# Optimization experiments

Measured on AMD Instinct MI355X. Metric: run time of the kernel, lower is better.

Reference implementation:

```python
import jax, jax.numpy as jnp
import numpy as np


def setup_inputs() -> dict:
    key = jax.random.key(0)
    k1, k2, k3 = jax.random.split(key, 3)
    B, N, C, H, W = 4, 6, 80, 16, 44
    image_features = jax.random.normal(k1, (B * N, C, H, W), dtype=jnp.float32)
    # eye + small perturbation keeps the 3x3 intrinsics block invertible
    intrinsics = jnp.eye(4, dtype=jnp.float32) + 0.1 * jax.random.normal(k2, (B, N, 4, 4), dtype=jnp.float32)
    extrinsics = jnp.eye(4, dtype=jnp.float32) + 0.1 * jax.random.normal(k3, (B, N, 4, 4), dtype=jnp.float32)
    return {"image_features": image_features, "intrinsics": intrinsics,
            "extrinsics": extrinsics, "depth_bins": 59}


def reference(image_features, intrinsics, extrinsics, depth_bins):
    BN, C, H, W = image_features.shape
    N = intrinsics.shape[1]
    B = BN // N
    dt = image_features.dtype
    depths = jnp.linspace(0.1, 1.0, depth_bins).astype(dt)  # (D,)
    feats = image_features.reshape(B, N, C, H, W)

    # pixel homogeneous coords, matching torch meshgrid(indexing='ij') + flatten
    yy, xx = jnp.meshgrid(jnp.arange(H), jnp.arange(W), indexing='ij')
    xy1 = jnp.stack([xx.ravel(), yy.ravel(), jnp.ones(H * W)], axis=0).astype(dt)  # (3, HW)

    K_inv = jnp.linalg.inv(intrinsics[:, :, :3, :3])            # (B,N,3,3)
    rays = jnp.einsum('bnij,jp->bnip', K_inv, xy1)              # (B,N,3,HW)

    # softmax over spatial dim (dim=3 of (B,N,C,HW) in the torch code)
    depth_probs = jax.nn.softmax(feats.reshape(B, N, C, H * W), axis=3)

    # In the original, only the LAST 4 channels of the (4C+1)-channel homogeneous
    # volume enter the extrinsic matmul: the [x,y,z] coords of channel C-1 plus 1.
    d_last = depth_probs[:, :, -1]                              # (B,N,HW)
    # (B,N,3,HW,D) = rays * (prob * depth)
    pts = rays[..., None] * (d_last[:, :, None, :, None] * depths)

    R = extrinsics[:, :, :3, :3]                                # (B,N,3,3)
    t = extrinsics[:, :, :3, 3]                                 # (B,N,3)
    world = jnp.einsum('bnij,bnjpd->bnipd', R, pts) + t[:, :, :, None, None]
    world = world.reshape(B, N, 3, H, W, depth_bins)

    feats_rep = jnp.broadcast_to(feats[..., None], (B, N, C, H, W, depth_bins))
    return jnp.concatenate([world, feats_rep], axis=2)         # (B,N,3+C,H,W,D)
```

## Files before the change

### kernel.cpp

```cpp
#include <hip/hip_runtime.h>


#define BB 4
#define NN 6
#define CC 80
#define HH 16
#define WW 44
#define DD 59
#define BN (BB*NN)
#define PP (HH*WW)
#define CHO (CC+3)
#define WD (WW*DD)

#define WS_DLAST (BN*12)

__device__ inline float waveMax(float v) {
#pragma unroll
    for (int o = 32; o; o >>= 1) v = fmaxf(v, __shfl_xor(v, o));
    return v;
}
__device__ inline float waveSum(float v) {
#pragma unroll
    for (int o = 32; o; o >>= 1) v += __shfl_xor(v, o);
    return v;
}

__global__ __launch_bounds__(256) void lss_prep(const float* __restrict__ feats,
                                                const float* __restrict__ intr,
                                                const float* __restrict__ extr,
                                                float* __restrict__ ws) {
    const int bn = blockIdx.x;
    const int tid = threadIdx.x;
    float* Mt = ws + bn * 12;
    float* dlast = ws + WS_DLAST + (size_t)bn * PP;
    const float* f = feats + ((size_t)bn * CC + (CC - 1)) * PP;

    __shared__ float sred[4];
    __shared__ float s_max, s_sum;

    float m = -1e30f;
    for (int p = tid; p < PP; p += 256) m = fmaxf(m, f[p]);
    m = waveMax(m);
    if ((tid & 63) == 0) sred[tid >> 6] = m;
    __syncthreads();
    if (tid == 0) s_max = fmaxf(fmaxf(sred[0], sred[1]), fmaxf(sred[2], sred[3]));
    __syncthreads();
    const float mm = s_max;

    float s = 0.f;
    for (int p = tid; p < PP; p += 256) s += expf(f[p] - mm);
    s = waveSum(s);
    if ((tid & 63) == 0) sred[tid >> 6] = s;
    __syncthreads();
    if (tid == 0) s_sum = sred[0] + sred[1] + sred[2] + sred[3];
    __syncthreads();
    const float inv = 1.0f / s_sum;

    for (int p = tid; p < PP; p += 256) dlast[p] = expf(f[p] - mm) * inv;

    if (tid == 0) {
        const float* K = intr + bn * 16;
        float a = K[0], b = K[1], c = K[2];
        float d = K[4], e = K[5], ff = K[6];
        float g = K[8], h = K[9], i = K[10];
        float det = a * (e * i - ff * h) - b * (d * i - ff * g) + c * (d * h - e * g);
        float id = 1.0f / det;
        float kinv[9] = {
            (e * i - ff * h) * id, (c * h - b * i) * id, (b * ff - c * e) * id,
            (ff * g - d * i) * id, (a * i - c * g) * id, (c * d - a * ff) * id,
            (d * h - e * g) * id,  (b * g - a * h) * id, (a * e - b * d) * id
        };
        const float* E = extr + bn * 16;
#pragma unroll
        for (int r = 0; r < 3; ++r) {
#pragma unroll
            for (int cc2 = 0; cc2 < 3; ++cc2) {
                float acc = 0.f;
#pragma unroll
                for (int k = 0; k < 3; ++k) acc += E[r * 4 + k] * kinv[k * 3 + cc2];
                Mt[r * 3 + cc2] = acc;
            }
            Mt[9 + r] = E[r * 4 + 3];
        }
    }
}

__global__ __launch_bounds__(256) void lss_write(const float* __restrict__ feats,
                                                 const float* __restrict__ ws,
                                                 float* __restrict__ out) {
    const int blk = blockIdx.x;
    const int h = blk & (HH - 1);
    const int chbn = blk >> 4;
    const int ch = chbn % CHO;
    const int bn = chbn / CHO;
    const int tid = threadIdx.x;

    __shared__ float valw[WW];
    __shared__ float s_t;

    const float* Mt = ws + bn * 12;
    const bool isWorld = (ch < 3);

    if (isWorld) {
        if (tid < WW) {
            const float* dlast = ws + WS_DLAST + (size_t)bn * PP + h * WW;
            float x = (float)tid, y = (float)h;
            float ray = Mt[ch * 3 + 0] * x + Mt[ch * 3 + 1] * y + Mt[ch * 3 + 2];
            valw[tid] = ray * dlast[tid];
        }
        if (tid == 0) s_t = Mt[9 + ch];
    } else {
        if (tid < WW) {
            const float* frow = feats + (((size_t)bn * CC + (ch - 3)) * HH + h) * WW;
            valw[tid] = frow[tid];
        }
        if (tid == 0) s_t = 0.f;
    }
    __syncthreads();

    const float tval = s_t;
    float4* orow = (float4*)(out + (size_t)blk * WD);

    for (int q = tid; q < WD / 4; q += 256) {
        int base = q * 4;
        int w = base / DD;
        int d = base - w * DD;
        float4 v;
        float* pv = &v.x;
#pragma unroll
        for (int k = 0; k < 4; ++k) {
            float val = valw[w];
            if (isWorld) val = val * (0.1f + d * (0.9f / 58.f)) + tval;
            pv[k] = val;
            if (++d == DD) { d = 0; ++w; }
        }
        orow[q] = v;
    }
}

extern "C" void kernel_launch(void* const* d_in, const int* in_sizes, int n_in,
                              void* d_out, int out_size, void* d_ws, size_t ws_size,
                              hipStream_t stream) {
    const float* feats = (const float*)d_in[0];
    const float* intr  = (const float*)d_in[1];
    const float* extr  = (const float*)d_in[2];
    float* ws  = (float*)d_ws;
    float* out = (float*)d_out;

    lss_prep<<<BN, 256, 0, stream>>>(feats, intr, extr, ws);
    lss_write<<<BN * CHO * HH, 256, 0, stream>>>(feats, ws, out);
}
```

Before: 78.67 us.

## Fuse prep and write kernels, recompute softmax per world block, use nontemporal stores

Merges the softmax/matrix prep kernel into the output-writing kernel. Each world-channel block recomputes the softmax of the last feature channel and its camera matrix row locally. Blocks now cover half the image rows instead of one row, and per-thread index/scale tables are precomputed once and reused across rows. Output goes out with nontemporal vector stores. The launch and the workspace round trip go away, at the cost of redundant softmax work in world blocks and fewer, larger blocks.

```diff
diff --git a/kernel.cpp b/kernel.cpp
--- a/kernel.cpp
+++ b/kernel.cpp
@@ -11,8 +11,12 @@
 #define PP (HH*WW)
 #define CHO (CC+3)
 #define WD (WW*DD)
+#define NQ4 (WD/4)
+#define HSPLIT 2
+#define HLOC (HH/HSPLIT)
+#define DSTEP (0.9f/58.f)
 
-#define WS_DLAST (BN*12)
+typedef float fx4 __attribute__((ext_vector_type(4)));
 
 __device__ inline float waveMax(float v) {
 #pragma unroll
@@ -25,116 +29,141 @@
     return v;
 }
 
-__global__ __launch_bounds__(256) void lss_prep(const float* __restrict__ feats,
-                                                const float* __restrict__ intr,
-                                                const float* __restrict__ extr,
-                                                float* __restrict__ ws) {
-    const int bn = blockIdx.x;
-    const int tid = threadIdx.x;
-    float* Mt = ws + bn * 12;
-    float* dlast = ws + WS_DLAST + (size_t)bn * PP;
-    const float* f = feats + ((size_t)bn * CC + (CC - 1)) * PP;
+__global__ __launch_bounds__(256) void lss_all(const float* __restrict__ feats,
+                                               const float* __restrict__ intr,
+                                               const float* __restrict__ extr,
+                                               float* __restrict__ out) {
+    const int blk  = blockIdx.x;
+    const int hs   = blk & (HSPLIT - 1);
+    const int chbn = blk >> 1;
+    const int ch   = chbn % CHO;
+    const int bn   = chbn / CHO;
+    const int tid  = threadIdx.x;
+    const bool world = (ch < 3);
 
+    __shared__ float sf[PP];
+    __shared__ float valw[HLOC][WW + 1];
     __shared__ float sred[4];
-    __shared__ float s_max, s_sum;
+    __shared__ float sbc[2];
 
-    float m = -1e30f;
-    for (int p = tid; p < PP; p += 256) m = fmaxf(m, f[p]);
-    m = waveMax(m);
-    if ((tid & 63) == 0) sred[tid >> 6] = m;
-    __syncthreads();
-    if (tid == 0) s_max = fmaxf(fmaxf(sred[0], sred[1]), fmaxf(sred[2], sred[3]));
-    __syncthreads();
-    const float mm = s_max;
+    float tval = 0.f;
 
-    float s = 0.f;
-    for (int p = tid; p < PP; p += 256) s += expf(f[p] - mm);
-    s = waveSum(s);
-    if ((tid & 63) == 0) sred[tid >> 6] = s;
-    __syncthreads();
-    if (tid == 0) s_sum = sred[0] + sred[1] + sred[2] + sred[3];
-    __syncthreads();
-    const float inv = 1.0f / s_sum;
+    if (world) {
+        const float* f = feats + ((size_t)bn * CC + (CC - 1)) * PP;
+        float m = -1e30f;
+        for (int p = tid; p < PP; p += 256) { float v = f[p]; sf[p] = v; m = fmaxf(m, v); }
+        m = waveMax(m);
+        if ((tid & 63) == 0) sred[tid >> 6] = m;
+        __syncthreads();
+        if (tid == 0) sbc[0] = fmaxf(fmaxf(sred[0], sred[1]), fmaxf(sred[2], sred[3]));
+        __syncthreads();
+        const float mm = sbc[0];
+        float s = 0.f;
+        for (int p = tid; p < PP; p += 256) { float e = expf(sf[p] - mm); sf[p] = e; s += e; }
+        s = waveSum(s);
+        if ((tid & 63) == 0) sred[tid >> 6] = s;
+        __syncthreads();
+        if (tid == 0) sbc[1] = sred[0] + sred[1] + sred[2] + sred[3];
+        __syncthreads();
+        const float inv = 1.0f / sbc[1];
 
-    for (int p = tid; p < PP; p += 256) dlast[p] = expf(f[p] - mm) * inv;
-
-    if (tid == 0) {
         const float* K = intr + bn * 16;
         float a = K[0], b = K[1], c = K[2];
         float d = K[4], e = K[5], ff = K[6];
-        float g = K[8], h = K[9], i = K[10];
-        float det = a * (e * i - ff * h) - b * (d * i - ff * g) + c * (d * h - e * g);
+        float g = K[8], h9 = K[9], i9 = K[10];
+        float det = a * (e * i9 - ff * h9) - b * (d * i9 - ff * g) + c * (d * h9 - e * g);
         float id = 1.0f / det;
         float kinv[9] = {
-            (e * i - ff * h) * id, (c * h - b * i) * id, (b * ff - c * e) * id,
-            (ff * g - d * i) * id, (a * i - c * g) * id, (c * d - a * ff) * id,
-            (d * h - e * g) * id,  (b * g - a * h) * id, (a * e - b * d) * id
+            (e * i9 - ff * h9) * id, (c * h9 - b * i9) * id, (b * ff - c * e) * id,
+            (ff * g - d * i9) * id,  (a * i9 - c * g) * id,  (c * d - a * ff) * id,
+            (d * h9 - e * g) * id,   (b * g - a * h9) * id,  (a * e - b * d) * id
         };
         const float* E = extr + bn * 16;
-#pragma unroll
-        for (int r = 0; r < 3; ++r) {
-#pragma unroll
-            for (int cc2 = 0; cc2 < 3; ++cc2) {
-                float acc = 0.f;
-#pragma unroll
-                for (int k = 0; k < 3; ++k) acc += E[r * 4 + k] * kinv[k * 3 + cc2];
-                Mt[r * 3 + cc2] = acc;
-            }
-            Mt[9 + r] = E[r * 4 + 3];
+        float M0 = E[ch * 4 + 0] * kinv[0] + E[ch * 4 + 1] * kinv[3] + E[ch * 4 + 2] * kinv[6];
+        float M1 = E[ch * 4 + 0] * kinv[1] + E[ch * 4 + 1] * kinv[4] + E[ch * 4 + 2] * kinv[7];
+        float M2 = E[ch * 4 + 0] * kinv[2] + E[ch * 4 + 1] * kinv[5] + E[ch * 4 + 2] * kinv[8];
+        tval = E[ch * 4 + 3];
+
+        for (int t2 = tid; t2 < HLOC * WW; t2 += 256) {
+            int hl = t2 / WW;
+            int w  = t2 - hl * WW;
+            int h  = hs * HLOC + hl;
+            float ray = M0 * (float)w + M1 * (float)h + M2;
+            valw[hl][w] = ray * sf[h * WW + w] * inv;
+        }
+    } else {
+        const float* frow = feats + ((size_t)bn * CC + (ch - 3)) * PP + hs * HLOC * WW;
+        for (int t2 = tid; t2 < HLOC * WW; t2 += 256) {
+            int hl = t2 / WW;
+            int w  = t2 - hl * WW;
+            valw[hl][w] = frow[t2];
         }
     }
-}
-
-__global__ __launch_bounds__(256) void lss_write(const float* __restrict__ feats,
-                                                 const float* __restrict__ ws,
-                                                 float* __restrict__ out) {
-    const int blk = blockIdx.x;
-    const int h = blk & (HH - 1);
-    const int chbn = blk >> 4;
-    const int ch = chbn % CHO;
-    const int bn = chbn / CHO;
-    const int tid = threadIdx.x;
-
-    __shared__ float valw[WW];
-    __shared__ float s_t;
-
-    const float* Mt = ws + bn * 12;
-    const bool isWorld = (ch < 3);
-
-    if (isWorld) {
-        if (tid < WW) {
-            const float* dlast = ws + WS_DLAST + (size_t)bn * PP + h * WW;
-            float x = (float)tid, y = (float)h;
-            float ray = Mt[ch * 3 + 0] * x + Mt[ch * 3 + 1] * y + Mt[ch * 3 + 2];
-            valw[tid] = ray * dlast[tid];
-        }
-        if (tid == 0) s_t = Mt[9 + ch];
-    } else {
-        if (tid < WW) {
-            const float* frow = feats + (((size_t)bn * CC + (ch - 3)) * HH + h) * WW;
-            valw[tid] = frow[tid];
-        }
-        if (tid == 0) s_t = 0.f;
-    }
+    if (tid < HLOC) valw[tid][WW] = 0.f;
     __syncthreads();
 
-    const float tval = s_t;
-    float4* orow = (float4*)(out + (size_t)blk * WD);
+    int   wA[3];
+    int   cross[3][4];
+    float sc[3][4];
+#pragma unroll
+    for (int i = 0; i < 3; ++i) {
+        int q = tid + 256 * i;
+        if (q < NQ4) {
+            int base = 4 * q;
+            int w    = base / DD;
+            int dlo  = base - DD * w;
+            wA[i] = w;
+#pragma unroll
+            for (int k = 0; k < 4; ++k) {
+                int dd   = dlo + k;
+                int cr   = (dd >= DD) ? 1 : 0;
+                int deff = dd - cr * DD;
+                cross[i][k] = cr;
+                sc[i][k] = 0.1f + (float)deff * DSTEP;
+            }
+        }
+    }
 
-    for (int q = tid; q < WD / 4; q += 256) {
-        int base = q * 4;
-        int w = base / DD;
-        int d = base - w * DD;
-        float4 v;
-        float* pv = &v.x;
+    float* obase = out + (((size_t)(bn * CHO + ch)) * HH + hs * HLOC) * WD;
+
+    if (world) {
+        for (int hl = 0; hl < HLOC; ++hl) {
+            const float* vr = valw[hl];
+            float* orow = obase + (size_t)hl * WD;
 #pragma unroll
-        for (int k = 0; k < 4; ++k) {
-            float val = valw[w];
-            if (isWorld) val = val * (0.1f + d * (0.9f / 58.f)) + tval;
-            pv[k] = val;
-            if (++d == DD) { d = 0; ++w; }
+            for (int i = 0; i < 3; ++i) {
+                int q = tid + 256 * i;
+                if (q < NQ4) {
+                    float v0 = vr[wA[i]];
+                    float v1 = vr[wA[i] + 1];
+                    fx4 r;
+                    r.x = (cross[i][0] ? v1 : v0) * sc[i][0] + tval;
+                    r.y = (cross[i][1] ? v1 : v0) * sc[i][1] + tval;
+                    r.z = (cross[i][2] ? v1 : v0) * sc[i][2] + tval;
+                    r.w = (cross[i][3] ? v1 : v0) * sc[i][3] + tval;
+                    __builtin_nontemporal_store(r, (fx4*)(orow + 4 * q));
+                }
+            }
         }
-        orow[q] = v;
+    } else {
+        for (int hl = 0; hl < HLOC; ++hl) {
+            const float* vr = valw[hl];
+            float* orow = obase + (size_t)hl * WD;
+#pragma unroll
+            for (int i = 0; i < 3; ++i) {
+                int q = tid + 256 * i;
+                if (q < NQ4) {
+                    float v0 = vr[wA[i]];
+                    float v1 = vr[wA[i] + 1];
+                    fx4 r;
+                    r.x = cross[i][0] ? v1 : v0;
+                    r.y = cross[i][1] ? v1 : v0;
+                    r.z = cross[i][2] ? v1 : v0;
+                    r.w = cross[i][3] ? v1 : v0;
+                    __builtin_nontemporal_store(r, (fx4*)(orow + 4 * q));
+                }
+            }
+        }
     }
 }
 
@@ -144,9 +173,7 @@
     const float* feats = (const float*)d_in[0];
     const float* intr  = (const float*)d_in[1];
     const float* extr  = (const float*)d_in[2];
-    float* ws  = (float*)d_ws;
     float* out = (float*)d_out;
 
-    lss_prep<<<BN, 256, 0, stream>>>(feats, intr, extr, ws);
-    lss_write<<<BN * CHO * HH, 256, 0, stream>>>(feats, ws, out);
+    lss_all<<<BN * CHO * HSPLIT, 256, 0, stream>>>(feats, intr, extr, out);
 }
```

After: 92.24 us. +17.2%, slower.
